# Performance work log

Hardware: AMD Instinct MI355X
Metric: run time of the kernel (lower is better)

Reference implementation:

```python
import jax, jax.numpy as jnp
import numpy as np

B, S, H = 2, 2048, 2048
NH, G = 16, 4
HD = H // NH  # 128


def setup_inputs() -> dict:
    key = jax.random.key(0)
    ks = jax.random.split(key, 9)
    sc = 0.02
    x = jax.random.normal(ks[0], (B, S, H), dtype=jnp.float32)
    # causal mask: 1.0 where j > i (masked), added as mask * -1e9 (matches torch code)
    causal_mask = jnp.triu(jnp.ones((S, S), dtype=jnp.float32), k=1)[None, None]
    Wq = jax.random.normal(ks[1], (H, H), dtype=jnp.float32) * sc
    bq = jnp.zeros((H,), dtype=jnp.float32)
    Wk = jax.random.normal(ks[2], (H, G * HD), dtype=jnp.float32) * sc
    bk = jnp.zeros((G * HD,), dtype=jnp.float32)
    Wv = jax.random.normal(ks[3], (H, G * HD), dtype=jnp.float32) * sc
    bv = jnp.zeros((G * HD,), dtype=jnp.float32)
    Wo = jax.random.normal(ks[4], (H, H), dtype=jnp.float32) * sc
    bo = jnp.zeros((H,), dtype=jnp.float32)
    return {"hidden_state": x, "causal_mask": causal_mask,
            "Wq": Wq, "bq": bq, "Wk": Wk, "bk": bk,
            "Wv": Wv, "bv": bv, "Wo": Wo, "bo": bo}


def reference(hidden_state, causal_mask, Wq, bq, Wk, bk, Wv, bv, Wo, bo):
    bsz, seq_len, _ = hidden_state.shape
    npg = NH // G  # query heads per KV group
    q = hidden_state @ Wq + bq                      # [B,S,H]
    k = hidden_state @ Wk + bk                      # [B,S,G*HD]
    v = hidden_state @ Wv + bv                      # [B,S,G*HD]
    # split heads; group query heads by KV group instead of repeating K/V
    q = q.reshape(bsz, seq_len, G, npg, HD).transpose(0, 2, 3, 1, 4)   # [B,G,npg,S,HD]
    k = k.reshape(bsz, seq_len, G, HD).transpose(0, 2, 1, 3)           # [B,G,S,HD]
    v = v.reshape(bsz, seq_len, G, HD).transpose(0, 2, 1, 3)           # [B,G,S,HD]
    scale = 1.0 / jnp.sqrt(jnp.float32(HD))
    scores = jnp.einsum('bgnsd,bgtd->bgnst', q, k) * scale             # [B,G,npg,S,S]
    scores = scores + causal_mask[:, :, None] * (-1e9)
    probs = jax.nn.softmax(scores, axis=-1)
    out = jnp.einsum('bgnst,bgtd->bgnsd', probs, v)                    # [B,G,npg,S,HD]
    out = out.transpose(0, 3, 1, 2, 4).reshape(bsz, seq_len, H)        # [B,S,H]
    return out @ Wo + bo
```

## Files before the change

### kernel.cpp

```cpp
#include <hip/hip_runtime.h>
#include <hip/hip_bf16.h>

#define B_   2
#define S_   2048
#define H_   2048
#define NH_  16
#define G_   4
#define HD_  128
#define NPG_ 4
#define MROWS_ (B_ * S_)
#define KVC_   (G_ * HD_)
#define NT_    (S_ / 64)
#define QSCALE_ 0.08838834764831845f

typedef __attribute__((ext_vector_type(8))) short bf16x8;
typedef __attribute__((ext_vector_type(4))) float f32x4;

__device__ __forceinline__ short f2bf_s(float f) {
    __hip_bfloat16 h = __float2bfloat16(f);
    short s; __builtin_memcpy(&s, &h, 2); return s;
}

__device__ __forceinline__ void gll16(const void* g, void* l) {
    __builtin_amdgcn_global_load_lds(
        (const __attribute__((address_space(1))) unsigned int*)g,
        (__attribute__((address_space(3))) unsigned int*)l, 16, 0, 0);
}

struct alignas(16) bf8pack { short s[8]; };
struct alignas(8)  s4pack  { short s[4]; };

__device__ __forceinline__ bf16x8 ld2x64(const short* p) {
    s4pack lo = *(const s4pack*)p;
    s4pack hi = *(const s4pack*)(p + 4);
    bf16x8 v;
    __builtin_memcpy(&v, &lo, 8);
    __builtin_memcpy((char*)&v + 8, &hi, 8);
    return v;
}

__device__ __forceinline__ void tile_transpose64(
    const float* __restrict__ in, __hip_bfloat16* __restrict__ out,
    int R, int C, int bx, int by, int tid) {
    __shared__ short tile[64][66];
    const int r = tid >> 2, c0 = (tid & 3) * 16;
    const float4* src = (const float4*)(in + (size_t)(by * 64 + r) * C + bx * 64 + c0);
    float4 f0 = src[0], f1 = src[1], f2 = src[2], f3 = src[3];
    short* tp = &tile[r][c0];
    tp[0]  = f2bf_s(f0.x); tp[1]  = f2bf_s(f0.y);
    tp[2]  = f2bf_s(f0.z); tp[3]  = f2bf_s(f0.w);
    tp[4]  = f2bf_s(f1.x); tp[5]  = f2bf_s(f1.y);
    tp[6]  = f2bf_s(f1.z); tp[7]  = f2bf_s(f1.w);
    tp[8]  = f2bf_s(f2.x); tp[9]  = f2bf_s(f2.y);
    tp[10] = f2bf_s(f2.z); tp[11] = f2bf_s(f2.w);
    tp[12] = f2bf_s(f3.x); tp[13] = f2bf_s(f3.y);
    tp[14] = f2bf_s(f3.z); tp[15] = f2bf_s(f3.w);
    __syncthreads();
    const int j = tid >> 2, i0 = (tid & 3) * 16;
    short pk[16];
    #pragma unroll
    for (int i = 0; i < 16; ++i) pk[i] = tile[i0 + i][j];
    __hip_bfloat16* dst = out + (size_t)(bx * 64 + j) * R + by * 64 + i0;
    *(uint4*)(dst)     = *(uint4*)(pk);
    *(uint4*)(dst + 8) = *(uint4*)(pk + 8);
}

__global__ __launch_bounds__(256) void prep(
    const float* __restrict__ x,  bf8pack* __restrict__ xb,
    const float* __restrict__ Wq, __hip_bfloat16* __restrict__ WqT,
    const float* __restrict__ Wk, __hip_bfloat16* __restrict__ WkT,
    const float* __restrict__ Wv, __hip_bfloat16* __restrict__ WvT,
    const float* __restrict__ Wo, __hip_bfloat16* __restrict__ WoT,
    const float* __restrict__ bq, const float* __restrict__ bk,
    const float* __restrict__ bv, float* __restrict__ bqkv) {
    const int bid = blockIdx.x, tid = threadIdx.x;
    if (bid < 4096) {
        int i = bid * 256 + tid;
        const float4* p = (const float4*)(x + (size_t)i * 8);
        float4 a = p[0], c = p[1];
        bf8pack o;
        o.s[0] = f2bf_s(a.x); o.s[1] = f2bf_s(a.y);
        o.s[2] = f2bf_s(a.z); o.s[3] = f2bf_s(a.w);
        o.s[4] = f2bf_s(c.x); o.s[5] = f2bf_s(c.y);
        o.s[6] = f2bf_s(c.z); o.s[7] = f2bf_s(c.w);
        xb[i] = o;
    } else if (bid < 5120) {
        int t = bid - 4096;
        tile_transpose64(Wq, WqT, H_, H_, t & 31, t >> 5, tid);
    } else if (bid < 5376) {
        int t = bid - 5120;
        tile_transpose64(Wk, WkT, H_, KVC_, t & 7, t >> 3, tid);
    } else if (bid < 5632) {
        int t = bid - 5376;
        tile_transpose64(Wv, WvT, H_, KVC_, t & 7, t >> 3, tid);
    } else if (bid < 6656) {
        int t = bid - 5632;
        tile_transpose64(Wo, WoT, H_, H_, t & 31, t >> 5, tid);
    } else {
        int i = (bid - 6656) * 256 + tid;
        if (i < 3072)
            bqkv[i] = (i < 2048) ? bq[i] : (i < 2560) ? bk[i - 2048] : bv[i - 2560];
    }
}

template <int BM, int NF>
__device__ __forceinline__ void gemm_core(
    const __hip_bfloat16* __restrict__ A,
    const __hip_bfloat16* __restrict__ Bt,
    const int K, const int bm, const int bn,
    short* __restrict__ As, short* __restrict__ Bs,
    f32x4 (* __restrict__ acc)[NF])
{
    constexpr int MH  = BM / 64;
    constexpr int AI  = BM / 64;
    constexpr int NB2 = NF - 2;
    constexpr int STG = AI + NF;
    constexpr int ASZ = BM * 64;
    constexpr int BSZ = 64 * NF * 64;
    const int t0 = threadIdx.x;
    const int lane = t0 & 63, wave = t0 >> 6;
    const int l15 = lane & 15, quad = lane >> 4;
    const int lrow = lane >> 3, lcg = lane & 7;
    const int wm = (wave >> 2) * (BM / 2);
    const int wn = (wave & 3) * (16 * NF);
    const int nt = K >> 6;

    auto stage = [&](int ti) {
        const int kt = ti << 6;
        short* Ad = As + (ti & 1) * ASZ;
        short* Bd = Bs + (ti & 1) * BSZ;
        #pragma unroll
        for (int p = 0; p < AI; ++p) {
            const int r0 = wave * (AI * 8) + p * 8;
            const int row = r0 + lrow;
            gll16(A + (size_t)(bm + row) * K + kt + ((lcg ^ (row & 7)) << 3),
                  Ad + r0 * 64);
        }
        #pragma unroll
        for (int p = 0; p < NF; ++p) {
            const int r0 = wave * (NF * 8) + p * 8;
            const int row = r0 + lrow;
            gll16(Bt + (size_t)(bn + row) * K + kt + ((lcg ^ (row & 7)) << 3),
                  Bd + r0 * 64);
        }
    };

    auto waitcnt_stg = [&]() {
        if constexpr (STG == 7)      asm volatile("s_waitcnt vmcnt(7)" ::: "memory");
        else if constexpr (STG == 6) asm volatile("s_waitcnt vmcnt(6)" ::: "memory");
        else if constexpr (STG == 8) asm volatile("s_waitcnt vmcnt(8)" ::: "memory");
        else                         asm volatile("s_waitcnt vmcnt(0)" ::: "memory");
    };

    stage(0); stage(1);
    waitcnt_stg();
    asm volatile("s_barrier" ::: "memory");

    for (int t = 0; t < nt; ++t) {
        const short* Ab = As + (t & 1) * ASZ;
        const short* Bb = Bs + (t & 1) * BSZ;
        bf16x8 bg1[2][2], bg2[NB2][2], ah[MH][2];

        #pragma unroll
        for (int n = 0; n < 2; ++n) {
            const int rb = wn + n * 16 + l15;
            #pragma unroll
            for (int ks = 0; ks < 2; ++ks)
                bg1[n][ks] = *(const bf16x8*)(Bb + rb * 64 +
                    (((ks * 4 + quad) ^ (rb & 7)) << 3));
        }
        #pragma unroll
        for (int i = 0; i < MH; ++i) {
            const int ra = wm + i * 16 + l15;
            #pragma unroll
            for (int ks = 0; ks < 2; ++ks)
                ah[i][ks] = *(const bf16x8*)(Ab + ra * 64 +
                    (((ks * 4 + quad) ^ (ra & 7)) << 3));
        }
        asm volatile("s_barrier" ::: "memory");
        asm volatile("s_waitcnt lgkmcnt(0)" ::: "memory");
        __builtin_amdgcn_s_setprio(1);
        #pragma unroll
        for (int ks = 0; ks < 2; ++ks)
            #pragma unroll
            for (int i = 0; i < MH; ++i)
                #pragma unroll
                for (int n = 0; n < 2; ++n)
                    acc[i][n] = __builtin_amdgcn_mfma_f32_16x16x32_bf16(
                        ah[i][ks], bg1[n][ks], acc[i][n], 0, 0, 0);
        __builtin_amdgcn_s_setprio(0);
        asm volatile("s_barrier" ::: "memory");

        #pragma unroll
        for (int n = 0; n < NB2; ++n) {
            const int rb = wn + (2 + n) * 16 + l15;
            #pragma unroll
            for (int ks = 0; ks < 2; ++ks)
                bg2[n][ks] = *(const bf16x8*)(Bb + rb * 64 +
                    (((ks * 4 + quad) ^ (rb & 7)) << 3));
        }
        asm volatile("s_barrier" ::: "memory");
        asm volatile("s_waitcnt lgkmcnt(0)" ::: "memory");
        __builtin_amdgcn_s_setprio(1);
        #pragma unroll
        for (int ks = 0; ks < 2; ++ks)
            #pragma unroll
            for (int i = 0; i < MH; ++i)
                #pragma unroll
                for (int n = 0; n < NB2; ++n)
                    acc[i][2 + n] = __builtin_amdgcn_mfma_f32_16x16x32_bf16(
                        ah[i][ks], bg2[n][ks], acc[i][2 + n], 0, 0, 0);
        __builtin_amdgcn_s_setprio(0);
        asm volatile("s_barrier" ::: "memory");

        #pragma unroll
        for (int i = 0; i < MH; ++i) {
            const int ra = wm + (MH + i) * 16 + l15;
            #pragma unroll
            for (int ks = 0; ks < 2; ++ks)
                ah[i][ks] = *(const bf16x8*)(Ab + ra * 64 +
                    (((ks * 4 + quad) ^ (ra & 7)) << 3));
        }
        asm volatile("s_barrier" ::: "memory");
        asm volatile("s_waitcnt lgkmcnt(0)" ::: "memory");
        __builtin_amdgcn_s_setprio(1);
        #pragma unroll
        for (int ks = 0; ks < 2; ++ks)
            #pragma unroll
            for (int i = 0; i < MH; ++i)
                #pragma unroll
                for (int n = 0; n < NB2; ++n)
                    acc[MH + i][2 + n] = __builtin_amdgcn_mfma_f32_16x16x32_bf16(
                        ah[i][ks], bg2[n][ks], acc[MH + i][2 + n], 0, 0, 0);
        __builtin_amdgcn_s_setprio(0);
        asm volatile("s_barrier" ::: "memory");

        if (t + 2 < nt) stage(t + 2);
        __builtin_amdgcn_s_setprio(1);
        #pragma unroll
        for (int ks = 0; ks < 2; ++ks)
            #pragma unroll
            for (int i = 0; i < MH; ++i)
                #pragma unroll
                for (int n = 0; n < 2; ++n)
                    acc[MH + i][n] = __builtin_amdgcn_mfma_f32_16x16x32_bf16(
                        ah[i][ks], bg1[n][ks], acc[MH + i][n], 0, 0, 0);
        __builtin_amdgcn_s_setprio(0);

        if (t + 2 < nt) {
            waitcnt_stg();
            asm volatile("s_barrier" ::: "memory");
        } else if (t + 1 < nt) {
            asm volatile("s_waitcnt vmcnt(0)" ::: "memory");
            asm volatile("s_barrier" ::: "memory");
        }
    }
}

__global__ __launch_bounds__(512, 2) void gemm_qkv8(
    const __hip_bfloat16* __restrict__ A,
    const __hip_bfloat16* __restrict__ Bt,
    const float* __restrict__ bias,
    __hip_bfloat16* __restrict__ Qo,
    __hip_bfloat16* __restrict__ Ko,
    __hip_bfloat16* __restrict__ VtG) {
    __shared__ __align__(16) short As[2 * 256 * 64];
    __shared__ __align__(16) short Bs[2 * 192 * 64];
    const int bid = blockIdx.x;
    const int s = (bid & 7) * 32 + (bid >> 3);
    const int bm = (s & 15) * 256, bn = (s >> 4) * 192;

    f32x4 acc[8][3] = {};
    gemm_core<256, 3>(A, Bt, H_, bm, bn, As, Bs, acc);

    const int t = threadIdx.x;
    const int lane = t & 63, wave = t >> 6;
    const int l15 = lane & 15, quad = lane >> 4;
    const int wm = (wave >> 2) * 128, wn = (wave & 3) * 48;

    #pragma unroll
    for (int i = 0; i < 8; ++i) {
        int row0 = bm + wm + i * 16 + quad * 4;
        #pragma unroll
        for (int j = 0; j < 3; ++j) {
            int c0 = bn + wn + j * 16;
            int colg = c0 + l15;
            float bv = bias[colg];
            if (c0 < 2048) {
                #pragma unroll
                for (int r = 0; r < 4; ++r)
                    Qo[(size_t)(row0 + r) * H_ + colg] =
                        __float2bfloat16((acc[i][j][r] + bv) * QSCALE_);
            } else if (c0 < 2560) {
                #pragma unroll
                for (int r = 0; r < 4; ++r)
                    Ko[(size_t)(row0 + r) * KVC_ + (colg - 2048)] =
                        __float2bfloat16(acc[i][j][r] + bv);
            } else {
                int coll = colg - 2560;
                short s4v[4];
                #pragma unroll
                for (int r = 0; r < 4; ++r) s4v[r] = f2bf_s(acc[i][j][r] + bv);
                *(uint2*)(&VtG[(size_t)coll * MROWS_ + row0]) = *(uint2*)s4v;
            }
        }
    }
}

__global__ __launch_bounds__(512, 2) void gemm_out8(
    const __hip_bfloat16* __restrict__ A,
    const __hip_bfloat16* __restrict__ Bt,
    const float* __restrict__ bias,
    float* __restrict__ C) {
    __shared__ __align__(16) short As[2 * 128 * 64];
    __shared__ __align__(16) short Bs[2 * 256 * 64];
    const int bid = blockIdx.x;
    const int s = (bid & 7) * 32 + (bid >> 3);
    const int bm = (s & 31) * 128, bn = (s >> 5) * 256;

    f32x4 acc[4][4] = {};
    gemm_core<128, 4>(A, Bt, H_, bm, bn, As, Bs, acc);

    const int t = threadIdx.x;
    const int lane = t & 63, wave = t >> 6;
    const int l15 = lane & 15, quad = lane >> 4;
    const int wm = (wave >> 2) * 64, wn = (wave & 3) * 64;

    #pragma unroll
    for (int i = 0; i < 4; ++i) {
        int row0 = bm + wm + i * 16 + quad * 4;
        #pragma unroll
        for (int j = 0; j < 4; ++j) {
            int col = bn + wn + j * 16 + l15;
            float bv = bias[col];
            #pragma unroll
            for (int r = 0; r < 4; ++r)
                C[(size_t)(row0 + r) * H_ + col] = acc[i][j][r] + bv;
        }
    }
}

__global__ __launch_bounds__(256, 2) void attn_causal_gqa(
    const __hip_bfloat16* __restrict__ Q,
    const __hip_bfloat16* __restrict__ K,
    const __hip_bfloat16* __restrict__ VtG,
    __hip_bfloat16* __restrict__ O) {
    __shared__ short KsL[2][64 * 128];
    __shared__ short VtL[128 * 64];
    __shared__ short Ps[4][2][16 * 76];

    const int h  = blockIdx.x;
    const int b  = h >> 4;
    const int hh = h & 15;
    const int g  = hh >> 2;
    const int qb1 = blockIdx.y;
    const int qb2 = NT_ - 1 - qb1;

    const int t = threadIdx.x;
    const int lane = t & 63, wave = t >> 6;
    const int l15 = lane & 15, quad = lane >> 4;
    const int swz = l15 & 7;

    const __hip_bfloat16* Qb = Q + (size_t)b * S_ * H_ + hh * HD_;
    const __hip_bfloat16* Kb = K + (size_t)b * S_ * KVC_ + g * HD_;
    const __hip_bfloat16* Vg = VtG + (size_t)g * HD_ * MROWS_ + b * S_;

    auto stageK = [&](int tile) {
        short* kd = &KsL[tile & 1][0];
        #pragma unroll
        for (int p = 0; p < 4; ++p) {
            int R0 = wave * 16 + p * 4;
            int row = R0 + (lane >> 4);
            int cg = ((lane & 15) ^ (row & 7)) * 8;
            gll16(Kb + (size_t)(tile * 64 + row) * KVC_ + cg, &kd[R0 * 128]);
        }
    };
    auto stageV = [&](int tile) {
        #pragma unroll
        for (int p = 0; p < 4; ++p) {
            int R0 = wave * 32 + p * 8;
            int row = R0 + (lane >> 3);
            int cg = ((lane & 7) ^ (row & 7)) * 8;
            gll16(Vg + (size_t)row * MROWS_ + tile * 64 + cg, &VtL[R0 * 64]);
        }
    };

    bf16x8 aq1[4], aq2[4];
    {
        const int qr1 = qb1 * 64 + wave * 16 + l15;
        const int qr2 = qb2 * 64 + wave * 16 + l15;
        #pragma unroll
        for (int kk = 0; kk < 4; ++kk) {
            aq1[kk] = *(const bf16x8*)(Qb + (size_t)qr1 * H_ + kk * 32 + quad * 8);
            aq2[kk] = *(const bf16x8*)(Qb + (size_t)qr2 * H_ + kk * 32 + quad * 8);
        }
    }

    f32x4 o1[8] = {}, o2[8] = {};
    float lp1 = 0.f, lp2 = 0.f;
    const int qrow_loc = wave * 16 + l15;

    stageK(0);

    for (int tile = 0; tile <= qb2; ++tile) {
        const bool do1 = (tile <= qb1);
        const bool last = (tile == qb2);

        stageV(tile);
        if (!last) stageK(tile + 1);

        if (!last) asm volatile("s_waitcnt vmcnt(8)" ::: "memory");
        else       asm volatile("s_waitcnt vmcnt(4)" ::: "memory");
        asm volatile("s_barrier" ::: "memory");

        const short* kb = &KsL[tile & 1][0];

        f32x4 s2[4] = {}, s1[4] = {};
        #pragma unroll
        for (int kk = 0; kk < 4; ++kk) {
            bf16x8 bk[4];
            #pragma unroll
            for (int nt = 0; nt < 4; ++nt)
                bk[nt] = *(const bf16x8*)(
                    &kb[(nt * 16 + l15) * 128 + (((kk * 4 + quad) ^ swz) * 8)]);
            #pragma unroll
            for (int nt = 0; nt < 4; ++nt)
                s2[nt] = __builtin_amdgcn_mfma_f32_16x16x32_bf16(
                    bk[nt], aq2[kk], s2[nt], 0, 0, 0);
            if (do1) {
                #pragma unroll
                for (int nt = 0; nt < 4; ++nt)
                    s1[nt] = __builtin_amdgcn_mfma_f32_16x16x32_bf16(
                        bk[nt], aq1[kk], s1[nt], 0, 0, 0);
            }
        }

        __asm__ volatile("" ::: "memory");
        short* P2 = &Ps[wave][1][0];
        {
            const bool m2 = (tile == qb2);
            #pragma unroll
            for (int nt = 0; nt < 4; ++nt) {
                s4pack pk;
                #pragma unroll
                for (int r = 0; r < 4; ++r) {
                    float p = __expf(s2[nt][r]);
                    if (m2 && (nt * 16 + quad * 4 + r > qrow_loc)) p = 0.f;
                    lp2 += p;
                    pk.s[r] = f2bf_s(p);
                }
                *(s4pack*)&P2[l15 * 76 + nt * 16 + quad * 4] = pk;
            }
        }
        short* P1 = &Ps[wave][0][0];
        if (do1) {
            const bool m1 = (tile == qb1);
            #pragma unroll
            for (int nt = 0; nt < 4; ++nt) {
                s4pack pk;
                #pragma unroll
                for (int r = 0; r < 4; ++r) {
                    float p = __expf(s1[nt][r]);
                    if (m1 && (nt * 16 + quad * 4 + r > qrow_loc)) p = 0.f;
                    lp1 += p;
                    pk.s[r] = f2bf_s(p);
                }
                *(s4pack*)&P1[l15 * 76 + nt * 16 + quad * 4] = pk;
            }
        }
        __asm__ volatile("" ::: "memory");

        if (!last) asm volatile("s_waitcnt vmcnt(4)" ::: "memory");
        else       asm volatile("s_waitcnt vmcnt(0)" ::: "memory");
        asm volatile("s_barrier" ::: "memory");

        #pragma unroll
        for (int ks = 0; ks < 2; ++ks) {
            bf16x8 ap2 = ld2x64(&P2[l15 * 76 + ks * 32 + quad * 8]);
            bf16x8 ap1;
            if (do1) ap1 = ld2x64(&P1[l15 * 76 + ks * 32 + quad * 8]);
            #pragma unroll
            for (int n2 = 0; n2 < 8; ++n2) {
                bf16x8 bv = *(const bf16x8*)(
                    &VtL[(n2 * 16 + l15) * 64 + (((ks * 4 + quad) ^ swz) * 8)]);
                o2[n2] = __builtin_amdgcn_mfma_f32_16x16x32_bf16(
                    ap2, bv, o2[n2], 0, 0, 0);
                if (do1)
                    o1[n2] = __builtin_amdgcn_mfma_f32_16x16x32_bf16(
                        ap1, bv, o1[n2], 0, 0, 0);
            }
        }
        asm volatile("s_barrier" ::: "memory");
    }

    float L1 = lp1, L2 = lp2;
    L1 += __shfl_xor(L1, 16); L2 += __shfl_xor(L2, 16);
    L1 += __shfl_xor(L1, 32); L2 += __shfl_xor(L2, 32);
    #pragma unroll
    for (int r = 0; r < 4; ++r) {
        float i1 = 1.f / __shfl(L1, quad * 4 + r);
        float i2 = 1.f / __shfl(L2, quad * 4 + r);
        int s1r = qb1 * 64 + wave * 16 + quad * 4 + r;
        int s2r = qb2 * 64 + wave * 16 + quad * 4 + r;
        #pragma unroll
        for (int n2 = 0; n2 < 8; ++n2) {
            int d = n2 * 16 + l15;
            O[((size_t)b * S_ + s1r) * H_ + hh * HD_ + d] = __float2bfloat16(o1[n2][r] * i1);
            O[((size_t)b * S_ + s2r) * H_ + hh * HD_ + d] = __float2bfloat16(o2[n2][r] * i2);
        }
    }
}

extern "C" void kernel_launch(void* const* d_in, const int* in_sizes, int n_in,
                              void* d_out, int out_size, void* d_ws, size_t ws_size,
                              hipStream_t stream) {
    const float* x  = (const float*)d_in[0];
    const float* Wq = (const float*)d_in[2];
    const float* bq = (const float*)d_in[3];
    const float* Wk = (const float*)d_in[4];
    const float* bk = (const float*)d_in[5];
    const float* Wv = (const float*)d_in[6];
    const float* bv = (const float*)d_in[7];
    const float* Wo = (const float*)d_in[8];
    const float* bo = (const float*)d_in[9];
    float* out = (float*)d_out;

    char* ws = (char*)d_ws;
    const size_t MB = 1024 * 1024;
    __hip_bfloat16* xb   = (__hip_bfloat16*)(ws);
    __hip_bfloat16* WT   = (__hip_bfloat16*)(ws + 16 * MB);
    __hip_bfloat16* Kws  = (__hip_bfloat16*)(ws + 28 * MB);
    __hip_bfloat16* VtG  = (__hip_bfloat16*)(ws + 32 * MB);
    __hip_bfloat16* WoT  = (__hip_bfloat16*)(ws + 36 * MB);
    float*          bqkv = (float*)         (ws + 44 * MB);
    __hip_bfloat16* Aws  = (__hip_bfloat16*)(ws);
    __hip_bfloat16* Qbuf = (__hip_bfloat16*)d_out;

    prep<<<6669, 256, 0, stream>>>(
        x, (bf8pack*)xb,
        Wq, WT,
        Wk, WT + (size_t)2048 * H_,
        Wv, WT + (size_t)2560 * H_,
        Wo, WoT,
        bq, bk, bv, bqkv);

    gemm_qkv8<<<256, 512, 0, stream>>>(xb, WT, bqkv, Qbuf, Kws, VtG);

    attn_causal_gqa<<<dim3(B_ * NH_, NT_ / 2), 256, 0, stream>>>(Qbuf, Kws, VtG, Aws);

    gemm_out8<<<256, 512, 0, stream>>>(Aws, WoT, bo, out);
}
```

Measured before the change: 303.8 us.

## Spread GEMM global-to-LDS loads across compute phases with finer-grained staging

The shared GEMM core now splits tile loading across the four MFMA phases of each k-step. The A tile for the next step is issued in two halves during the first two phases. The B tile for two steps ahead is issued in two halves during the last two phases. The end-of-step wait only drains the A loads and leaves part of the B loads in flight. The goal is to smooth memory traffic and overlap it better with MFMA work, in exchange for a more intricate wait-count scheme and a shorter prefetch distance for A.

```diff
diff --git a/kernel.cpp b/kernel.cpp
--- a/kernel.cpp
+++ b/kernel.cpp
@@ -95,7 +95,7 @@
         tile_transpose64(Wv, WvT, H_, KVC_, t & 7, t >> 3, tid);
     } else if (bid < 6656) {
         int t = bid - 5632;
-        tile_transpose64(Wo, WoT, H_, H_, t & 31, t >> 5, tid);
+        tile_transpose64(Wo, WoT, H_, H_, t & 63 & 31, (t >> 5), tid);
     } else {
         int i = (bid - 6656) * 256 + tid;
         if (i < 3072)
@@ -104,7 +104,7 @@
 }
 
 template <int BM, int NF>
-__device__ __forceinline__ void gemm_core(
+__device__ __forceinline__ void gemm8(
     const __hip_bfloat16* __restrict__ A,
     const __hip_bfloat16* __restrict__ Bt,
     const int K, const int bm, const int bn,
@@ -112,9 +112,8 @@
     f32x4 (* __restrict__ acc)[NF])
 {
     constexpr int MH  = BM / 64;
-    constexpr int AI  = BM / 64;
+    constexpr int AHL = BM / 128;
     constexpr int NB2 = NF - 2;
-    constexpr int STG = AI + NF;
     constexpr int ASZ = BM * 64;
     constexpr int BSZ = 64 * NF * 64;
     const int t0 = threadIdx.x;
@@ -125,35 +124,41 @@
     const int wn = (wave & 3) * (16 * NF);
     const int nt = K >> 6;
 
-    auto stage = [&](int ti) {
+    auto stageAh = [&](int ti, int h) {
         const int kt = ti << 6;
         short* Ad = As + (ti & 1) * ASZ;
-        short* Bd = Bs + (ti & 1) * BSZ;
-        #pragma unroll
-        for (int p = 0; p < AI; ++p) {
-            const int r0 = wave * (AI * 8) + p * 8;
+        #pragma unroll
+        for (int p = 0; p < AHL; ++p) {
+            const int r0 = h * (BM / 2) + wave * (8 * AHL) + p * 8;
             const int row = r0 + lrow;
             gll16(A + (size_t)(bm + row) * K + kt + ((lcg ^ (row & 7)) << 3),
                   Ad + r0 * 64);
         }
-        #pragma unroll
-        for (int p = 0; p < NF; ++p) {
-            const int r0 = wave * (NF * 8) + p * 8;
-            const int row = r0 + lrow;
-            gll16(Bt + (size_t)(bn + row) * K + kt + ((lcg ^ (row & 7)) << 3),
-                  Bd + r0 * 64);
-        }
     };
-
-    auto waitcnt_stg = [&]() {
-        if constexpr (STG == 7)      asm volatile("s_waitcnt vmcnt(7)" ::: "memory");
-        else if constexpr (STG == 6) asm volatile("s_waitcnt vmcnt(6)" ::: "memory");
-        else if constexpr (STG == 8) asm volatile("s_waitcnt vmcnt(8)" ::: "memory");
-        else                         asm volatile("s_waitcnt vmcnt(0)" ::: "memory");
+    auto stageBu = [&](int ti, int u) {
+        const int kt = ti << 6;
+        short* Bd = Bs + (ti & 1) * BSZ;
+        const int r0 = u * 64 + wave * 8;
+        const int row = r0 + lrow;
+        gll16(Bt + (size_t)(bn + row) * K + kt + ((lcg ^ (row & 7)) << 3),
+              Bd + r0 * 64);
     };
-
-    stage(0); stage(1);
-    waitcnt_stg();
+    auto wait_nf = [&]() {
+        if constexpr (NF == 3) asm volatile("s_waitcnt vmcnt(3)" ::: "memory");
+        else if constexpr (NF == 4) asm volatile("s_waitcnt vmcnt(4)" ::: "memory");
+        else asm volatile("s_waitcnt vmcnt(0)" ::: "memory");
+    };
+
+    stageAh(0, 0); stageAh(0, 1);
+    #pragma unroll
+    for (int u = 0; u < NF; ++u) stageBu(0, u);
+    if (nt > 1) {
+        #pragma unroll
+        for (int u = 0; u < NF; ++u) stageBu(1, u);
+        wait_nf();
+    } else {
+        asm volatile("s_waitcnt vmcnt(0)" ::: "memory");
+    }
     asm volatile("s_barrier" ::: "memory");
 
     for (int t = 0; t < nt; ++t) {
@@ -177,6 +182,7 @@
                 ah[i][ks] = *(const bf16x8*)(Ab + ra * 64 +
                     (((ks * 4 + quad) ^ (ra & 7)) << 3));
         }
+        if (t + 1 < nt) stageAh(t + 1, 0);
         asm volatile("s_barrier" ::: "memory");
         asm volatile("s_waitcnt lgkmcnt(0)" ::: "memory");
         __builtin_amdgcn_s_setprio(1);
@@ -199,6 +205,7 @@
                 bg2[n][ks] = *(const bf16x8*)(Bb + rb * 64 +
                     (((ks * 4 + quad) ^ (rb & 7)) << 3));
         }
+        if (t + 1 < nt) stageAh(t + 1, 1);
         asm volatile("s_barrier" ::: "memory");
         asm volatile("s_waitcnt lgkmcnt(0)" ::: "memory");
         __builtin_amdgcn_s_setprio(1);
@@ -221,6 +228,10 @@
                 ah[i][ks] = *(const bf16x8*)(Ab + ra * 64 +
                     (((ks * 4 + quad) ^ (ra & 7)) << 3));
         }
+        if (t + 2 < nt) {
+            #pragma unroll
+            for (int u = 0; u < NF / 2; ++u) stageBu(t + 2, u);
+        }
         asm volatile("s_barrier" ::: "memory");
         asm volatile("s_waitcnt lgkmcnt(0)" ::: "memory");
         __builtin_amdgcn_s_setprio(1);
@@ -235,7 +246,10 @@
         __builtin_amdgcn_s_setprio(0);
         asm volatile("s_barrier" ::: "memory");
 
-        if (t + 2 < nt) stage(t + 2);
+        if (t + 2 < nt) {
+            #pragma unroll
+            for (int u = NF / 2; u < NF; ++u) stageBu(t + 2, u);
+        }
         __builtin_amdgcn_s_setprio(1);
         #pragma unroll
         for (int ks = 0; ks < 2; ++ks)
@@ -247,13 +261,9 @@
                         ah[i][ks], bg1[n][ks], acc[MH + i][n], 0, 0, 0);
         __builtin_amdgcn_s_setprio(0);
 
-        if (t + 2 < nt) {
-            waitcnt_stg();
-            asm volatile("s_barrier" ::: "memory");
-        } else if (t + 1 < nt) {
-            asm volatile("s_waitcnt vmcnt(0)" ::: "memory");
-            asm volatile("s_barrier" ::: "memory");
-        }
+        if (t + 2 < nt) wait_nf();
+        else            asm volatile("s_waitcnt vmcnt(0)" ::: "memory");
+        asm volatile("s_barrier" ::: "memory");
     }
 }
 
@@ -271,7 +281,7 @@
     const int bm = (s & 15) * 256, bn = (s >> 4) * 192;
 
     f32x4 acc[8][3] = {};
-    gemm_core<256, 3>(A, Bt, H_, bm, bn, As, Bs, acc);
+    gemm8<256, 3>(A, Bt, H_, bm, bn, As, Bs, acc);
 
     const int t = threadIdx.x;
     const int lane = t & 63, wave = t >> 6;
@@ -319,7 +329,7 @@
     const int bm = (s & 31) * 128, bn = (s >> 5) * 256;
 
     f32x4 acc[4][4] = {};
-    gemm_core<128, 4>(A, Bt, H_, bm, bn, As, Bs, acc);
+    gemm8<128, 4>(A, Bt, H_, bm, bn, As, Bs, acc);
 
     const int t = threadIdx.x;
     const int lane = t & 63, wave = t >> 6;
```

Result: slower. 312.2 us (+2.8%).
